# Optimization experiments

Hardware: AMD Instinct MI355X
Metric: run time of the kernel (lower is better)

Reference implementation:

```python
import jax, jax.numpy as jnp
import numpy as np

B, C, H, W = 32, 3, 480, 640
_GRAY_W = jnp.array([0.299, 0.587, 0.114], dtype=jnp.float32)  # torchvision rgb_to_grayscale weights


def _blend(img1, img2, ratio):
    # torchvision _blend for float images: clamp to [0, 1]
    return jnp.clip(ratio * img1 + (1.0 - ratio) * img2, 0.0, 1.0)


def _rgb_to_gray(x):
    # x: [B,3,H,W] -> [B,1,H,W]
    return jnp.einsum('bchw,c->bhw', x, _GRAY_W)[:, None]


def _adjust_hue(x, hf):
    # x: [B,3,H,W] in [0,1], hf: [B] hue shift. RGB->HSV, h += hf (mod 1), HSV->RGB.
    r, g, b = x[:, 0], x[:, 1], x[:, 2]
    maxc = jnp.max(x, axis=1)
    minc = jnp.min(x, axis=1)
    v = maxc
    cr = maxc - minc
    eqc = cr == 0
    crd = jnp.where(eqc, 1.0, cr)
    s = cr / jnp.where(maxc == 0, 1.0, maxc)
    rc = (maxc - r) / crd
    gc = (maxc - g) / crd
    bc = (maxc - b) / crd
    hr = jnp.where(maxc == r, bc - gc, 0.0)
    hg = jnp.where((maxc == g) & (maxc != r), 2.0 + rc - bc, 0.0)
    hb = jnp.where((maxc != g) & (maxc != r), 4.0 + gc - rc, 0.0)
    h = ((hr + hg + hb) / 6.0) % 1.0
    h = (h + hf[:, None, None]) % 1.0
    # HSV -> RGB
    i6 = h * 6.0
    i = jnp.floor(i6)
    f = i6 - i
    i = i.astype(jnp.int32) % 6
    p = v * (1.0 - s)
    q = v * (1.0 - f * s)
    t = v * (1.0 - (1.0 - f) * s)

    def sel(a0, a1, a2, a3, a4, a5):
        return jnp.select([i == 0, i == 1, i == 2, i == 3, i == 4], [a0, a1, a2, a3, a4], a5)

    r2 = sel(v, q, p, p, t, v)
    g2 = sel(t, v, v, q, p, p)
    b2 = sel(p, p, t, v, v, q)
    return jnp.stack([r2, g2, b2], axis=1)


def setup_inputs() -> dict:
    key = jax.random.key(0)
    k0, k1, k2, k3, k4 = jax.random.split(key, 5)
    x = jax.random.uniform(k0, (B, C, H, W), dtype=jnp.float32)
    brightness_f = jax.random.uniform(k1, (B,), minval=0.7, maxval=1.3, dtype=jnp.float32)
    contrast_f = jax.random.uniform(k2, (B,), minval=0.7, maxval=1.3, dtype=jnp.float32)
    saturation_f = jax.random.uniform(k3, (B,), minval=0.7, maxval=1.3, dtype=jnp.float32)
    hue_f = jax.random.uniform(k4, (B,), minval=-0.3, maxval=0.3, dtype=jnp.float32)
    return {"x": x, "brightness_f": brightness_f, "contrast_f": contrast_f,
            "saturation_f": saturation_f, "hue_f": hue_f, "num_samples": 1}


def reference(x, brightness_f, contrast_f, saturation_f, hue_f, num_samples):
    # Replicate each image num_samples times along batch -> [B*N, 3, H, W]
    x = jnp.repeat(x, num_samples, axis=0)
    bf = brightness_f[:, None, None, None]
    cf = contrast_f[:, None, None, None]
    sf = saturation_f[:, None, None, None]
    # brightness: blend with zeros
    x = jnp.clip(x * bf, 0.0, 1.0)
    # contrast: blend with per-image mean of grayscale
    gray = _rgb_to_gray(x)
    mean = jnp.mean(gray, axis=(2, 3), keepdims=True)
    x = _blend(x, mean, cf)
    # saturation: blend with grayscale of current image
    x = _blend(x, _rgb_to_gray(x), sf)
    # hue shift via HSV roundtrip
    x = _adjust_hue(x, hue_f)
    return x
```

## Files before the change

### kernel.cpp

```cpp
#include <hip/hip_runtime.h>

#define HW    307200
#define HW4   76800
#define CHW   921600
#define RED_BPB 60

__global__ __launch_bounds__(256) void cr_reduce_gray(
    const float* __restrict__ x,
    const float* __restrict__ bright,
    double* __restrict__ mean_ws,
    int ns)
{
    int b   = blockIdx.x / RED_BPB;
    int blk = blockIdx.x % RED_BPB;
    int b_in = (ns == 1) ? b : (b / ns);

    const float4* rp = (const float4*)(x + (size_t)b_in * CHW);
    const float4* gp = rp + HW4;
    const float4* bp = gp + HW4;
    float bf = bright[b];

    float acc = 0.0f;
    for (int p = blk * 256 + threadIdx.x; p < HW4; p += RED_BPB * 256) {
        float4 r = rp[p];
        float4 g = gp[p];
        float4 bl = bp[p];
        #pragma unroll
        for (int k = 0; k < 4; ++k) {
            float rr = fminf(fmaxf(((const float*)&r)[k]  * bf, 0.0f), 1.0f);
            float gg = fminf(fmaxf(((const float*)&g)[k]  * bf, 0.0f), 1.0f);
            float bb = fminf(fmaxf(((const float*)&bl)[k] * bf, 0.0f), 1.0f);
            acc += 0.299f * rr + 0.587f * gg + 0.114f * bb;
        }
    }

    #pragma unroll
    for (int off = 32; off > 0; off >>= 1)
        acc += __shfl_down(acc, off);

    __shared__ float wsum[4];
    int lane = threadIdx.x & 63;
    int wave = threadIdx.x >> 6;
    if (lane == 0) wsum[wave] = acc;
    __syncthreads();
    if (threadIdx.x == 0) {
        float s = wsum[0] + wsum[1] + wsum[2] + wsum[3];
        atomicAdd(&mean_ws[b], (double)s);
    }
}

__device__ __forceinline__ void cr_process(
    float r, float g, float b,
    float bf, float cf, float sf, float hf, float mean,
    float& ro, float& go, float& bo)
{
    r = fminf(fmaxf(r * bf, 0.0f), 1.0f);
    g = fminf(fmaxf(g * bf, 0.0f), 1.0f);
    b = fminf(fmaxf(b * bf, 0.0f), 1.0f);
    float omc = 1.0f - cf;
    r = fminf(fmaxf(cf * r + omc * mean, 0.0f), 1.0f);
    g = fminf(fmaxf(cf * g + omc * mean, 0.0f), 1.0f);
    b = fminf(fmaxf(cf * b + omc * mean, 0.0f), 1.0f);
    float gray = 0.299f * r + 0.587f * g + 0.114f * b;
    float oms = 1.0f - sf;
    r = fminf(fmaxf(sf * r + oms * gray, 0.0f), 1.0f);
    g = fminf(fmaxf(sf * g + oms * gray, 0.0f), 1.0f);
    b = fminf(fmaxf(sf * b + oms * gray, 0.0f), 1.0f);

    float maxc = fmaxf(r, fmaxf(g, b));
    float minc = fminf(r, fminf(g, b));
    float v  = maxc;
    float cr = maxc - minc;
    float crd = (cr == 0.0f) ? 1.0f : cr;
    float invcrd = 1.0f / crd;
    float md = (maxc == 0.0f) ? 1.0f : maxc;
    float s = cr / md;
    float rc = (maxc - r) * invcrd;
    float gc = (maxc - g) * invcrd;
    float bc = (maxc - b) * invcrd;

    float h = (maxc == r) ? (bc - gc)
            : ((maxc == g) ? (2.0f + rc - bc)
                           : (4.0f + gc - rc));
    h = h * (1.0f / 6.0f);
    h = h - floorf(h);
    h = h + hf;
    h = h - floorf(h);

    float i6 = h * 6.0f;
    float fi = floorf(i6);
    float f  = i6 - fi;
    int i = ((int)fi) % 6;

    float p = v * (1.0f - s);
    float q = v * (1.0f - f * s);
    float t = v * (1.0f - (1.0f - f) * s);

    ro = (i == 0 || i == 5) ? v : (i == 1 ? q : (i == 4 ? t : p));
    go = (i == 1 || i == 2) ? v : (i == 0 ? t : (i == 3 ? q : p));
    bo = (i == 3 || i == 4) ? v : (i == 5 ? q : (i == 2 ? t : p));
}

__global__ __launch_bounds__(256) void cr_apply(
    const float* __restrict__ x,
    const float* __restrict__ bright,
    const float* __restrict__ contrast,
    const float* __restrict__ sat,
    const float* __restrict__ hue,
    const double* __restrict__ mean_ws,
    float* __restrict__ out,
    int ns, int n)
{
    int idx = blockIdx.x * blockDim.x + threadIdx.x;
    if (idx >= n) return;
    int b  = idx / HW4;
    int p4 = idx - b * HW4;
    int b_in = (ns == 1) ? b : (b / ns);

    const float4* rp = (const float4*)(x + (size_t)b_in * CHW);
    const float4* gp = rp + HW4;
    const float4* bp = gp + HW4;
    float4* orp = (float4*)(out + (size_t)b * CHW);
    float4* ogp = orp + HW4;
    float4* obp = ogp + HW4;

    float bf = bright[b];
    float cf = contrast[b];
    float sf = sat[b];
    float hf = hue[b];
    float mean = (float)(mean_ws[b] * (1.0 / (double)HW));

    float4 r = rp[p4];
    float4 g = gp[p4];
    float4 bl = bp[p4];
    float4 ro, go, bo;

    cr_process(r.x, g.x, bl.x, bf, cf, sf, hf, mean, ro.x, go.x, bo.x);
    cr_process(r.y, g.y, bl.y, bf, cf, sf, hf, mean, ro.y, go.y, bo.y);
    cr_process(r.z, g.z, bl.z, bf, cf, sf, hf, mean, ro.z, go.z, bo.z);
    cr_process(r.w, g.w, bl.w, bf, cf, sf, hf, mean, ro.w, go.w, bo.w);

    orp[p4] = ro;
    ogp[p4] = go;
    obp[p4] = bo;
}

extern "C" void kernel_launch(void* const* d_in, const int* in_sizes, int n_in,
                              void* d_out, int out_size, void* d_ws, size_t ws_size,
                              hipStream_t stream) {
    const float* x  = (const float*)d_in[0];
    const float* bf = (const float*)d_in[1];
    const float* cf = (const float*)d_in[2];
    const float* sf = (const float*)d_in[3];
    const float* hf = (const float*)d_in[4];
    float* out = (float*)d_out;

    int ns = out_size / in_sizes[0];
    if (ns < 1) ns = 1;
    int B_out = out_size / CHW;

    double* mean_ws = (double*)d_ws;
    hipMemsetAsync(mean_ws, 0, (size_t)B_out * sizeof(double), stream);

    cr_reduce_gray<<<dim3(B_out * RED_BPB), dim3(256), 0, stream>>>(
        x, bf, mean_ws, ns);

    int n = B_out * HW4;
    cr_apply<<<dim3((n + 255) / 256), dim3(256), 0, stream>>>(
        x, bf, cf, sf, hf, mean_ws, out, ns, n);
}
```

Measured before the change: 231.3 us.

## Replace double atomics and memset with per-block partials reduced in apply kernel

The reduction kernel now writes one float partial sum per block instead of doing double-precision atomicAdd, which removes the memset launch and atomic contention. The apply kernel reduces the 60 partials per image in shared memory at block start and uses a 2D block-to-image mapping so no integer division per thread is needed. It also unrolls the fixed-trip reduction loop, precomputes blend constants, and uses nontemporal stores for the output. Summing in float instead of double slightly changes precision, and each apply block pays a small extra reduction plus a barrier.

```diff
diff --git a/kernel.cpp b/kernel.cpp
--- a/kernel.cpp
+++ b/kernel.cpp
@@ -1,35 +1,42 @@
 #include <hip/hip_runtime.h>
 
-#define HW    307200
-#define HW4   76800
-#define CHW   921600
+#define HW      307200
+#define HW4     76800
+#define CHW     921600
 #define RED_BPB 60
+#define APP_BPB 300
+
+typedef float vfloat4 __attribute__((ext_vector_type(4)));
+
+struct RGB { float r, g, b; };
 
 __global__ __launch_bounds__(256) void cr_reduce_gray(
     const float* __restrict__ x,
     const float* __restrict__ bright,
-    double* __restrict__ mean_ws,
+    float* __restrict__ part_ws,
     int ns)
 {
     int b   = blockIdx.x / RED_BPB;
     int blk = blockIdx.x % RED_BPB;
     int b_in = (ns == 1) ? b : (b / ns);
 
-    const float4* rp = (const float4*)(x + (size_t)b_in * CHW);
-    const float4* gp = rp + HW4;
-    const float4* bp = gp + HW4;
+    const vfloat4* rp = (const vfloat4*)(x + (size_t)b_in * CHW);
+    const vfloat4* gp = rp + HW4;
+    const vfloat4* bp = gp + HW4;
     float bf = bright[b];
 
     float acc = 0.0f;
-    for (int p = blk * 256 + threadIdx.x; p < HW4; p += RED_BPB * 256) {
-        float4 r = rp[p];
-        float4 g = gp[p];
-        float4 bl = bp[p];
+    #pragma unroll
+    for (int it = 0; it < 5; ++it) {
+        int p = blk * 256 + threadIdx.x + it * (RED_BPB * 256);
+        vfloat4 r  = rp[p];
+        vfloat4 g  = gp[p];
+        vfloat4 bl = bp[p];
         #pragma unroll
         for (int k = 0; k < 4; ++k) {
-            float rr = fminf(fmaxf(((const float*)&r)[k]  * bf, 0.0f), 1.0f);
-            float gg = fminf(fmaxf(((const float*)&g)[k]  * bf, 0.0f), 1.0f);
-            float bb = fminf(fmaxf(((const float*)&bl)[k] * bf, 0.0f), 1.0f);
+            float rr = fminf(fmaxf(r[k]  * bf, 0.0f), 1.0f);
+            float gg = fminf(fmaxf(g[k]  * bf, 0.0f), 1.0f);
+            float bb = fminf(fmaxf(bl[k] * bf, 0.0f), 1.0f);
             acc += 0.299f * rr + 0.587f * gg + 0.114f * bb;
         }
     }
@@ -43,29 +50,25 @@
     int wave = threadIdx.x >> 6;
     if (lane == 0) wsum[wave] = acc;
     __syncthreads();
-    if (threadIdx.x == 0) {
-        float s = wsum[0] + wsum[1] + wsum[2] + wsum[3];
-        atomicAdd(&mean_ws[b], (double)s);
-    }
+    if (threadIdx.x == 0)
+        part_ws[b * RED_BPB + blk] = wsum[0] + wsum[1] + wsum[2] + wsum[3];
 }
 
-__device__ __forceinline__ void cr_process(
+__device__ __forceinline__ RGB cr_process(
     float r, float g, float b,
-    float bf, float cf, float sf, float hf, float mean,
-    float& ro, float& go, float& bo)
+    float bf, float cf, float sf, float hf, float cmean)
 {
     r = fminf(fmaxf(r * bf, 0.0f), 1.0f);
     g = fminf(fmaxf(g * bf, 0.0f), 1.0f);
     b = fminf(fmaxf(b * bf, 0.0f), 1.0f);
-    float omc = 1.0f - cf;
-    r = fminf(fmaxf(cf * r + omc * mean, 0.0f), 1.0f);
-    g = fminf(fmaxf(cf * g + omc * mean, 0.0f), 1.0f);
-    b = fminf(fmaxf(cf * b + omc * mean, 0.0f), 1.0f);
+    r = fminf(fmaxf(cf * r + cmean, 0.0f), 1.0f);
+    g = fminf(fmaxf(cf * g + cmean, 0.0f), 1.0f);
+    b = fminf(fmaxf(cf * b + cmean, 0.0f), 1.0f);
     float gray = 0.299f * r + 0.587f * g + 0.114f * b;
-    float oms = 1.0f - sf;
-    r = fminf(fmaxf(sf * r + oms * gray, 0.0f), 1.0f);
-    g = fminf(fmaxf(sf * g + oms * gray, 0.0f), 1.0f);
-    b = fminf(fmaxf(sf * b + oms * gray, 0.0f), 1.0f);
+    float oms = (1.0f - sf) * gray;
+    r = fminf(fmaxf(sf * r + oms, 0.0f), 1.0f);
+    g = fminf(fmaxf(sf * g + oms, 0.0f), 1.0f);
+    b = fminf(fmaxf(sf * b + oms, 0.0f), 1.0f);
 
     float maxc = fmaxf(r, fmaxf(g, b));
     float minc = fminf(r, fminf(g, b));
@@ -96,9 +99,11 @@
     float q = v * (1.0f - f * s);
     float t = v * (1.0f - (1.0f - f) * s);
 
-    ro = (i == 0 || i == 5) ? v : (i == 1 ? q : (i == 4 ? t : p));
-    go = (i == 1 || i == 2) ? v : (i == 0 ? t : (i == 3 ? q : p));
-    bo = (i == 3 || i == 4) ? v : (i == 5 ? q : (i == 2 ? t : p));
+    RGB o;
+    o.r = (i == 0 || i == 5) ? v : (i == 1 ? q : (i == 4 ? t : p));
+    o.g = (i == 1 || i == 2) ? v : (i == 0 ? t : (i == 3 ? q : p));
+    o.b = (i == 3 || i == 4) ? v : (i == 5 ? q : (i == 2 ? t : p));
+    return o;
 }
 
 __global__ __launch_bounds__(256) void cr_apply(
@@ -107,42 +112,54 @@
     const float* __restrict__ contrast,
     const float* __restrict__ sat,
     const float* __restrict__ hue,
-    const double* __restrict__ mean_ws,
+    const float* __restrict__ part_ws,
     float* __restrict__ out,
-    int ns, int n)
+    int ns)
 {
-    int idx = blockIdx.x * blockDim.x + threadIdx.x;
-    if (idx >= n) return;
-    int b  = idx / HW4;
-    int p4 = idx - b * HW4;
+    int b    = blockIdx.x / APP_BPB;
+    int pblk = blockIdx.x % APP_BPB;
+    int p4   = pblk * 256 + threadIdx.x;
     int b_in = (ns == 1) ? b : (b / ns);
 
-    const float4* rp = (const float4*)(x + (size_t)b_in * CHW);
-    const float4* gp = rp + HW4;
-    const float4* bp = gp + HW4;
-    float4* orp = (float4*)(out + (size_t)b * CHW);
-    float4* ogp = orp + HW4;
-    float4* obp = ogp + HW4;
+    __shared__ float smean;
+    if (threadIdx.x < 64) {
+        float v = (threadIdx.x < RED_BPB) ? part_ws[b * RED_BPB + threadIdx.x] : 0.0f;
+        #pragma unroll
+        for (int off = 32; off > 0; off >>= 1)
+            v += __shfl_down(v, off);
+        if (threadIdx.x == 0) smean = v * (1.0f / (float)HW);
+    }
+    __syncthreads();
+
+    const vfloat4* rp = (const vfloat4*)(x + (size_t)b_in * CHW);
+    const vfloat4* gp = rp + HW4;
+    const vfloat4* bp = gp + HW4;
+    vfloat4* orp = (vfloat4*)(out + (size_t)b * CHW);
+    vfloat4* ogp = orp + HW4;
+    vfloat4* obp = ogp + HW4;
 
     float bf = bright[b];
     float cf = contrast[b];
     float sf = sat[b];
     float hf = hue[b];
-    float mean = (float)(mean_ws[b] * (1.0 / (double)HW));
+    float cmean = (1.0f - cf) * smean;
 
-    float4 r = rp[p4];
-    float4 g = gp[p4];
-    float4 bl = bp[p4];
-    float4 ro, go, bo;
+    vfloat4 r  = rp[p4];
+    vfloat4 g  = gp[p4];
+    vfloat4 bl = bp[p4];
+    vfloat4 ro, go, bo;
 
-    cr_process(r.x, g.x, bl.x, bf, cf, sf, hf, mean, ro.x, go.x, bo.x);
-    cr_process(r.y, g.y, bl.y, bf, cf, sf, hf, mean, ro.y, go.y, bo.y);
-    cr_process(r.z, g.z, bl.z, bf, cf, sf, hf, mean, ro.z, go.z, bo.z);
-    cr_process(r.w, g.w, bl.w, bf, cf, sf, hf, mean, ro.w, go.w, bo.w);
+    #pragma unroll
+    for (int k = 0; k < 4; ++k) {
+        RGB o = cr_process(r[k], g[k], bl[k], bf, cf, sf, hf, cmean);
+        ro[k] = o.r;
+        go[k] = o.g;
+        bo[k] = o.b;
+    }
 
-    orp[p4] = ro;
-    ogp[p4] = go;
-    obp[p4] = bo;
+    __builtin_nontemporal_store(ro, &orp[p4]);
+    __builtin_nontemporal_store(go, &ogp[p4]);
+    __builtin_nontemporal_store(bo, &obp[p4]);
 }
 
 extern "C" void kernel_launch(void* const* d_in, const int* in_sizes, int n_in,
@@ -159,13 +176,11 @@
     if (ns < 1) ns = 1;
     int B_out = out_size / CHW;
 
-    double* mean_ws = (double*)d_ws;
-    hipMemsetAsync(mean_ws, 0, (size_t)B_out * sizeof(double), stream);
+    float* part_ws = (float*)d_ws;
 
     cr_reduce_gray<<<dim3(B_out * RED_BPB), dim3(256), 0, stream>>>(
-        x, bf, mean_ws, ns);
+        x, bf, part_ws, ns);
 
-    int n = B_out * HW4;
-    cr_apply<<<dim3((n + 255) / 256), dim3(256), 0, stream>>>(
-        x, bf, cf, sf, hf, mean_ws, out, ns, n);
+    cr_apply<<<dim3(B_out * APP_BPB), dim3(256), 0, stream>>>(
+        x, bf, cf, sf, hf, part_ws, out, ns);
 }
```

New measurement: 227.0 us. Within noise of the previous version (-1.9%).
